# Optimization experiments

Hardware: AMD Instinct MI355X
Metric: run time of the kernel (lower is better)

The kernel has to match this reference:

```python
import jax, jax.numpy as jnp
import numpy as np
from jax import lax

B, C, H, W = 16, 3, 512, 512


def _nms(heat):
    # 3x3 max-pool, stride 1, SAME padding; keep only local peaks
    hmax = lax.reduce_window(heat, -jnp.inf, lax.max,
                             (1, 1, 3, 3), (1, 1, 1, 1), 'SAME')
    return heat * (hmax == heat).astype(heat.dtype)


def _topk(scores, K):
    b, c, h, w = scores.shape
    # per-class topk over the spatial plane
    topk_scores, topk_inds = lax.top_k(scores.reshape(b, c, h * w), K)  # [b,c,K]
    topk_row = (topk_inds // w).astype(scores.dtype)
    topk_col = (topk_inds % w).astype(scores.dtype)
    # global topk across (class, K)
    topk_score, topk_ind = lax.top_k(topk_scores.reshape(b, c * K), K)  # [b,K]
    topk_clses = topk_ind // K
    gath = lambda x: jnp.take_along_axis(x.reshape(b, c * K), topk_ind, axis=1)
    return topk_score, gath(topk_inds), topk_clses, gath(topk_row), gath(topk_col)


def _transpose_and_gather_feat(feat, inds):
    b, ch, h, w = feat.shape
    f = feat.transpose(0, 2, 3, 1).reshape(b, h * w, ch)  # [b,HW,ch]
    return jnp.take_along_axis(f, inds[:, :, None], axis=1)  # [b,K,ch]


def _decode(hm, cen_offset, direction, z_coor, dim, K):
    b = hm.shape[0]
    hm = _nms(hm)
    scores, inds, clses, row, col = _topk(hm, K)
    off = _transpose_and_gather_feat(cen_offset, inds)           # [b,K,2]
    col = col[:, :, None] + off[:, :, 0:1]
    row = row[:, :, None] + off[:, :, 1:2]
    direction = _transpose_and_gather_feat(direction, inds)      # [b,K,2]
    z_coor = _transpose_and_gather_feat(z_coor, inds)            # [b,K,1]
    dim = _transpose_and_gather_feat(dim, inds)                  # [b,K,3]
    clses = clses[:, :, None].astype(hm.dtype)
    scores = scores[:, :, None]
    return jnp.concatenate([scores, col, row, z_coor, dim, direction, clses], axis=2)


def setup_inputs() -> dict:
    key = jax.random.key(0)
    k1, k2, k3, k4, k5 = jax.random.split(key, 5)
    return {
        'hm_cen': jax.random.normal(k1, (B, C, H, W), jnp.float32),
        'cen_offset': jax.random.normal(k2, (B, 2, H, W), jnp.float32),
        'direction': jax.random.normal(k3, (B, 2, H, W), jnp.float32),
        'z_coor': jax.random.normal(k4, (B, 1, H, W), jnp.float32),
        'dim': jax.random.normal(k5, (B, 3, H, W), jnp.float32),
        'K': 500,
    }


def reference(hm_cen, cen_offset, direction, z_coor, dim, K):
    # postprocessing_v2 applies sigmoid to the class heatmap before decode
    heat = jax.nn.sigmoid(hm_cen)
    return _decode(heat, cen_offset, direction, z_coor, dim, K)  # [B,K,10]
```

## Files before the change

### kernel.cpp

```cpp
#include <hip/hip_runtime.h>
#include <math.h>
#include <float.h>

#define Hd 512
#define Wd 512
#define HWp (Hd*Wd)
#define Bn 16
#define Cn 3
#define NMAP (Bn*Cn)
#define KTOP 500
#define P_SPLIT 8
#define BAND 64
#define SCAP 4096

__device__ __forceinline__ uint32_t flipbits(float v){
  uint32_t u = __float_as_uint(v);
  return u ^ (0x80000000u | (uint32_t)(-(int32_t)(u>>31)));
}
__device__ __forceinline__ float unflipbits(uint32_t f){
  uint32_t u = f ^ ((f>>31)? 0x80000000u : 0xFFFFFFFFu);
  return __uint_as_float(u);
}

__device__ __forceinline__ void nms_row(
    const float4 p0, const float4 p1, const float4 c0, const float4 c1,
    const float4 n0, const float4 n1, const int lane,
    uint32_t& pk, float* cv)
{
  float vm0 = fmaxf(fmaxf(p0.x,c0.x),n0.x);
  float vm1 = fmaxf(fmaxf(p0.y,c0.y),n0.y);
  float vm2 = fmaxf(fmaxf(p0.z,c0.z),n0.z);
  float vm3 = fmaxf(fmaxf(p0.w,c0.w),n0.w);
  float vm4 = fmaxf(fmaxf(p1.x,c1.x),n1.x);
  float vm5 = fmaxf(fmaxf(p1.y,c1.y),n1.y);
  float vm6 = fmaxf(fmaxf(p1.z,c1.z),n1.z);
  float vm7 = fmaxf(fmaxf(p1.w,c1.w),n1.w);
  float vmL = __shfl_up(vm7, 1);   if (lane == 0)  vmL = -INFINITY;
  float vmR = __shfl_down(vm0, 1); if (lane == 63) vmR = -INFINITY;

  float m0 = fmaxf(vmL, fmaxf(vm0, vm1));
  float m1 = fmaxf(vm0, fmaxf(vm1, vm2));
  float m2 = fmaxf(vm1, fmaxf(vm2, vm3));
  float m3 = fmaxf(vm2, fmaxf(vm3, vm4));
  float m4 = fmaxf(vm3, fmaxf(vm4, vm5));
  float m5 = fmaxf(vm4, fmaxf(vm5, vm6));
  float m6 = fmaxf(vm5, fmaxf(vm6, vm7));
  float m7 = fmaxf(vm6, fmaxf(vm7, vmR));

  pk = 0;
  if (c0.x >= m0) pk |= 1u;
  if (c0.y >= m1) pk |= 2u;
  if (c0.z >= m2) pk |= 4u;
  if (c0.w >= m3) pk |= 8u;
  if (c1.x >= m4) pk |= 16u;
  if (c1.y >= m5) pk |= 32u;
  if (c1.z >= m6) pk |= 64u;
  if (c1.w >= m7) pk |= 128u;
  cv[0]=c0.x; cv[1]=c0.y; cv[2]=c0.z; cv[3]=c0.w;
  cv[4]=c1.x; cv[5]=c1.y; cv[6]=c1.z; cv[7]=c1.w;
}

__device__ __forceinline__ void append_row(
    const uint32_t pk, const float* cv, const uint32_t ibase,
    uint32_t* __restrict__ ctr, uint64_t* __restrict__ dst, const uint32_t cap,
    uint32_t* __restrict__ hist, const int lane)
{
  const uint32_t np = (uint32_t)__popc(pk);
  uint32_t incl = np;
  #pragma unroll
  for (int d = 1; d < 64; d <<= 1) { uint32_t u = __shfl_up(incl, d); if (lane >= d) incl += u; }
  const uint32_t tot = __shfl(incl, 63);
  if (!tot) return;
  uint32_t b0 = 0;
  if (lane == 0) b0 = atomicAdd(ctr, tot);
  b0 = __shfl(b0, 0);
  uint32_t pos = b0 + incl - np;
  #pragma unroll
  for (int i = 0; i < 8; ++i) {
    if ((pk >> i) & 1u) {
      const uint32_t fb = flipbits(cv[i]);
      if (pos < cap) dst[pos] = ((uint64_t)fb << 32) | (uint32_t)(~(ibase + (uint32_t)i));
      atomicAdd(&hist[fb >> 22], 1u);
      ++pos;
    }
  }
}

__device__ __forceinline__ void findT512(
    const uint32_t* hist, const uint32_t target, const int tid, const int lane,
    const int wid, uint32_t* wtot, uint32_t* res)
{
  const uint32_t s = hist[2*tid] + hist[2*tid+1];
  uint32_t v = s;
  #pragma unroll
  for (int d = 1; d < 64; d <<= 1) { uint32_t u = __shfl_down(v, d); if (lane + d < 64) v += u; }
  if (lane == 0) wtot[wid] = v;
  __syncthreads();
  uint32_t above = 0;
  for (int ww = wid + 1; ww < 8; ++ww) above += wtot[ww];
  const uint32_t gsuf = v + above;
  if (gsuf >= target && (gsuf - s) < target) {
    uint32_t cum = gsuf - s;
    for (int b = 2*tid + 1; b >= 2*tid; --b) {
      cum += hist[b];
      if (cum >= target) { res[0]=(uint32_t)b; res[1]=target-(cum-hist[b]); res[2]=cum; break; }
    }
  }
  __syncthreads();
}

__device__ __forceinline__ uint64_t cexch(uint64_t mine, uint64_t part, bool wantMax) {
  uint64_t mx = mine > part ? mine : part;
  uint64_t mn = mine > part ? part : mine;
  return wantMax ? mx : mn;
}

__device__ void bitonic512_reg(uint64_t& e0, uint64_t* sbuf, int tid, int lane)
{
  for (int k = 2; k <= 512; k <<= 1) {
    for (int j = k >> 1; j > 0; j >>= 1) {
      const bool up = ((tid & k) == 0);
      if (j >= 64) {
        __syncthreads();
        sbuf[tid] = e0;
        __syncthreads();
        uint64_t q = sbuf[tid ^ j];
        e0 = cexch(e0, q, up == ((tid & j) == 0));
      } else {
        uint64_t q = __shfl_xor((unsigned long long)e0, j);
        e0 = cexch(e0, q, up == ((lane & j) == 0));
      }
    }
  }
  __syncthreads();
  sbuf[tid] = e0;
  __syncthreads();
}

__device__ void sort1024_lds(uint64_t* a, int tid)
{
  for (int k = 2; k <= 1024; k <<= 1) {
    for (int j = k >> 1; j > 0; j >>= 1) {
      __syncthreads();
      const int lj = 31 - __clz(j);
      const int i  = ((tid >> lj) << (lj + 1)) | (tid & (j - 1));
      const int ixj = i | j;
      const uint64_t x = a[i], y = a[ixj];
      const bool up = ((i & k) == 0);
      const bool sw = up ? (x < y) : (x > y);
      if (sw) { a[i] = y; a[ixj] = x; }
    }
  }
  __syncthreads();
}

__global__ __launch_bounds__(512) void k_fused(
    const float* __restrict__ hm, uint64_t* __restrict__ l500)
{
  __shared__ uint64_t sbuf[SCAP];
  __shared__ uint32_t hist[1024];
  __shared__ uint32_t wtot[8];
  __shared__ uint32_t res[4];
  __shared__ uint32_t cnt1, cnt2;

  const int m = blockIdx.x >> 3, p = blockIdx.x & (P_SPLIT - 1);
  const int tid = threadIdx.x, lane = tid & 63, w = tid >> 6;
  const uint64_t lt = (1ull << lane) - 1ull;
  const float* map = hm + (size_t)m * HWp;
  const int xb = lane * 8;

  for (int i = tid; i < 1024; i += 512) hist[i] = 0;
  if (tid == 0) { cnt1 = 0; cnt2 = 0; }
  __syncthreads();

  const float4 NEG4 = make_float4(-INFINITY,-INFINITY,-INFINITY,-INFINITY);
  #pragma unroll
  for (int sub = 0; sub < 2; ++sub) {
    const int y0 = p * BAND + w * 8 + sub * 4;
    float4 ra[6], rb[6];
    #pragma unroll
    for (int r = 0; r < 6; ++r) {
      const int yy = y0 - 1 + r;
      if (yy >= 0 && yy < Hd) {
        const float* rp = map + (size_t)yy * Wd + xb;
        ra[r] = *(const float4*)rp; rb[r] = *(const float4*)(rp + 4);
      } else { ra[r] = NEG4; rb[r] = NEG4; }
    }
    #pragma unroll
    for (int r = 0; r < 4; ++r) {
      uint32_t pk; float cv[8];
      nms_row(ra[r], rb[r], ra[r+1], rb[r+1], ra[r+2], rb[r+2], lane, pk, cv);
      append_row(pk, cv, (uint32_t)((y0 + r) * Wd + xb), &cnt1, sbuf, (uint32_t)SCAP, hist, lane);
    }
  }
  __syncthreads();
  const uint32_t n = cnt1;
  const uint32_t nc = (n < (uint32_t)SCAP) ? n : (uint32_t)SCAP;

  uint32_t thresh20 = 0;
  if (n > 512) {
    findT512(hist, KTOP, tid, lane, w, wtot, res);
    const uint32_t T1 = res[0], krem = res[1];
    for (int i = tid; i < 1024; i += 512) hist[i] = 0;
    __syncthreads();
    #pragma unroll
    for (int s = 0; s < SCAP/512; ++s) {
      const uint32_t i = (uint32_t)tid + s * 512u;
      if (i < nc) {
        const uint32_t f = (uint32_t)(sbuf[i] >> 32);
        if ((f >> 22) == T1) atomicAdd(&hist[(f >> 12) & 1023u], 1u);
      }
    }
    __syncthreads();
    findT512(hist, krem, tid, lane, w, wtot, res);
    thresh20 = (T1 << 10) | res[0];
  }

  uint64_t sk0,sk1,sk2,sk3,sk4,sk5,sk6,sk7;
  bool kp0,kp1,kp2,kp3,kp4,kp5,kp6,kp7;
  {
    const uint32_t i0=(uint32_t)tid, i1=i0+512u, i2=i0+1024u, i3=i0+1536u,
                   i4=i0+2048u, i5=i0+2560u, i6=i0+3072u, i7=i0+3584u;
    sk0=sbuf[i0]; sk1=sbuf[i1]; sk2=sbuf[i2]; sk3=sbuf[i3];
    sk4=sbuf[i4]; sk5=sbuf[i5]; sk6=sbuf[i6]; sk7=sbuf[i7];
    kp0=(i0<nc)&&((uint32_t)(sk0>>44)>=thresh20);
    kp1=(i1<nc)&&((uint32_t)(sk1>>44)>=thresh20);
    kp2=(i2<nc)&&((uint32_t)(sk2>>44)>=thresh20);
    kp3=(i3<nc)&&((uint32_t)(sk3>>44)>=thresh20);
    kp4=(i4<nc)&&((uint32_t)(sk4>>44)>=thresh20);
    kp5=(i5<nc)&&((uint32_t)(sk5>>44)>=thresh20);
    kp6=(i6<nc)&&((uint32_t)(sk6>>44)>=thresh20);
    kp7=(i7<nc)&&((uint32_t)(sk7>>44)>=thresh20);
  }
  __syncthreads();
  #define APPEND1(SK, KP) {                                              \
    const unsigned long long mask = __ballot(KP);                        \
    if (mask) {                                                          \
      uint32_t b = 0;                                                    \
      if (lane == 0) b = atomicAdd(&cnt2, (uint32_t)__popcll(mask));     \
      b = __shfl(b, 0);                                                  \
      if (KP) {                                                          \
        const uint32_t pp = b + (uint32_t)__popcll(mask & lt);           \
        if (pp < 1024u) sbuf[pp] = SK;                                   \
      }                                                                  \
    }                                                                    \
  }
  APPEND1(sk0,kp0) APPEND1(sk1,kp1) APPEND1(sk2,kp2) APPEND1(sk3,kp3)
  APPEND1(sk4,kp4) APPEND1(sk5,kp5) APPEND1(sk6,kp6) APPEND1(sk7,kp7)
  #undef APPEND1
  __syncthreads();
  uint32_t M = cnt2; if (M > 1024u) M = 1024u;

  if (M <= 512u) {
    uint64_t e0 = (tid < (int)M) ? sbuf[tid] : 0ull;
    bitonic512_reg(e0, sbuf, tid, lane);
  } else {
    for (int i = (int)M + tid; i < 1024; i += 512) sbuf[i] = 0ull;
    sort1024_lds(sbuf, tid);
  }

  l500[(size_t)blockIdx.x * 512 + tid] = sbuf[tid];
}

__global__ __launch_bounds__(1024) void k_merge(
    const uint64_t* __restrict__ l500,
    float* __restrict__ s1_scores, uint32_t* __restrict__ s1_inds)
{
  __shared__ uint64_t ld[P_SPLIT * 512];
  const int m = blockIdx.x >> 1, h = blockIdx.x & 1;
  const int tid = threadIdx.x;
  const uint64_t* src = l500 + (size_t)m * (P_SPLIT * 512);
  for (int i = tid; i < P_SPLIT * 512; i += 1024) ld[i] = src[i];
  __syncthreads();

  #pragma unroll
  for (int e = 0; e < 2; ++e) {
    const int i = h * 2048 + e * 1024 + tid;
    const uint64_t kk = ld[i];
    const int r = i & 511, L = i >> 9;
    if (kk != 0ull && r < KTOP) {
      uint32_t pos[P_SPLIT - 1];
      #pragma unroll
      for (int d = 0; d < P_SPLIT - 1; ++d) pos[d] = 0;
      #pragma unroll
      for (int s = 512; s >= 1; s >>= 1) {
        #pragma unroll
        for (int d = 0; d < P_SPLIT - 1; ++d) {
          const uint64_t* lst = ld + (((L + 1 + d) & (P_SPLIT - 1)) << 9);
          const uint32_t idx = pos[d] + (uint32_t)s - 1u;
          const uint64_t v = (idx < 512u) ? lst[idx] : 0ull;
          if (v > kk) pos[d] += (uint32_t)s;
        }
      }
      uint32_t rank = (uint32_t)r;
      #pragma unroll
      for (int d = 0; d < P_SPLIT - 1; ++d) rank += pos[d];
      if (rank < KTOP) {
        const float v = unflipbits((uint32_t)(kk >> 32));
        s1_scores[m * 512 + rank] = 1.0f / (1.0f + expf(-v));
        s1_inds [m * 512 + rank] = ~(uint32_t)kk;
      }
    }
  }
}

__global__ __launch_bounds__(512) void k_final(
    const float* __restrict__ s1_scores, const uint32_t* __restrict__ s1_inds,
    const float* __restrict__ cen_offset, const float* __restrict__ direction,
    const float* __restrict__ z_coor, const float* __restrict__ dimf,
    float* __restrict__ out)
{
  __shared__ float ssc[Cn][KTOP];
  const int b = blockIdx.x / Cn, c = blockIdx.x % Cn;
  const int tid = threadIdx.x;

  for (int i = tid; i < Cn * KTOP; i += 512) {
    int cc = i / KTOP, r = i - cc * KTOP;
    ssc[cc][r] = s1_scores[(b * Cn + cc) * 512 + r];
  }
  __syncthreads();

  if (tid < KTOP) {
    const int r = tid;
    const int i = c * KTOP + r;
    const uint64_t mykey = ((uint64_t)flipbits(ssc[c][r]) << 32) | (uint32_t)(~(uint32_t)i);
    int rank = r;
    #pragma unroll
    for (int cd = 1; cd < Cn; ++cd) {
      const int cc = (c + cd) % Cn;
      int lo = 0, hi = KTOP;
      while (lo < hi) {
        int mid = (lo + hi) >> 1;
        uint64_t k2 = ((uint64_t)flipbits(ssc[cc][mid]) << 32)
                    | (uint32_t)(~(uint32_t)(cc * KTOP + mid));
        if (k2 > mykey) lo = mid + 1; else hi = mid;
      }
      rank += lo;
    }
    if (rank < KTOP) {
      const float* co = cen_offset + (size_t)b * 2 * HWp;
      const float* di = direction  + (size_t)b * 2 * HWp;
      const float* zc = z_coor     + (size_t)b * HWp;
      const float* dm = dimf       + (size_t)b * 3 * HWp;
      const int bcx = b * Cn + c;
      const uint32_t ind = s1_inds[bcx * 512 + r];
      float o[10];
      o[0] = ssc[c][r];
      o[1] = (float)(ind & (Wd - 1)) + co[ind];
      o[2] = (float)(ind >> 9) + co[HWp + ind];
      o[3] = zc[ind];
      o[4] = dm[ind];
      o[5] = dm[HWp + ind];
      o[6] = dm[2 * HWp + ind];
      o[7] = di[ind];
      o[8] = di[HWp + ind];
      o[9] = (float)c;
      float* op = out + ((size_t)b * KTOP + rank) * 10;
      #pragma unroll
      for (int q = 0; q < 10; ++q) op[q] = o[q];
    }
  }
}

extern "C" void kernel_launch(void* const* d_in, const int* in_sizes, int n_in,
                              void* d_out, int out_size, void* d_ws, size_t ws_size,
                              hipStream_t stream)
{
  const float* hm         = (const float*)d_in[0];
  const float* cen_offset = (const float*)d_in[1];
  const float* direction  = (const float*)d_in[2];
  const float* z_coor     = (const float*)d_in[3];
  const float* dimf       = (const float*)d_in[4];
  float* out = (float*)d_out;

  char* ws = (char*)d_ws;
  uint64_t* l500  = (uint64_t*)ws;
  size_t o1       = (size_t)NMAP * P_SPLIT * 512 * 8;
  float*    s1_sc = (float*)(ws + o1);
  uint32_t* s1_id = (uint32_t*)(ws + o1 + (size_t)NMAP * 512 * 4);

  k_fused<<<NMAP * P_SPLIT, 512, 0, stream>>>(hm, l500);
  k_merge<<<NMAP * 2, 1024, 0, stream>>>(l500, s1_sc, s1_id);
  k_final<<<Bn * Cn, 512, 0, stream>>>(s1_sc, s1_id, cen_offset, direction, z_coor, dimf, out);
}
```

Baseline: 51.43 us.

## Double k_fused block to 1024 threads and skip second histogram pass when possible

The fused NMS/top-k kernel now runs 1024 threads per block, each wave handling 4 rows instead of two 4-row sub-bands, which doubles the threads available to hide load latency. The threshold search can stop after the first 10-bit histogram when at most 1024 candidates survive. Otherwise a finer 12-bit second histogram is built. The candidate sort becomes a register/shuffle bitonic sort of up to 2048 elements, replacing the LDS-only 1024 sort. In exchange the block uses more shared memory (a 4096-bin histogram) and may sort larger candidate sets.

```diff
diff --git a/kernel.cpp b/kernel.cpp
--- a/kernel.cpp
+++ b/kernel.cpp
@@ -60,48 +60,41 @@
   cv[4]=c1.x; cv[5]=c1.y; cv[6]=c1.z; cv[7]=c1.w;
 }
 
-__device__ __forceinline__ void append_row(
-    const uint32_t pk, const float* cv, const uint32_t ibase,
-    uint32_t* __restrict__ ctr, uint64_t* __restrict__ dst, const uint32_t cap,
-    uint32_t* __restrict__ hist, const int lane)
-{
-  const uint32_t np = (uint32_t)__popc(pk);
-  uint32_t incl = np;
-  #pragma unroll
-  for (int d = 1; d < 64; d <<= 1) { uint32_t u = __shfl_up(incl, d); if (lane >= d) incl += u; }
-  const uint32_t tot = __shfl(incl, 63);
-  if (!tot) return;
-  uint32_t b0 = 0;
-  if (lane == 0) b0 = atomicAdd(ctr, tot);
-  b0 = __shfl(b0, 0);
-  uint32_t pos = b0 + incl - np;
-  #pragma unroll
-  for (int i = 0; i < 8; ++i) {
-    if ((pk >> i) & 1u) {
-      const uint32_t fb = flipbits(cv[i]);
-      if (pos < cap) dst[pos] = ((uint64_t)fb << 32) | (uint32_t)(~(ibase + (uint32_t)i));
-      atomicAdd(&hist[fb >> 22], 1u);
-      ++pos;
-    }
-  }
-}
-
-__device__ __forceinline__ void findT512(
+__device__ __forceinline__ void findT1024(
     const uint32_t* hist, const uint32_t target, const int tid, const int lane,
     const int wid, uint32_t* wtot, uint32_t* res)
 {
-  const uint32_t s = hist[2*tid] + hist[2*tid+1];
+  const uint32_t s = hist[tid];
   uint32_t v = s;
   #pragma unroll
   for (int d = 1; d < 64; d <<= 1) { uint32_t u = __shfl_down(v, d); if (lane + d < 64) v += u; }
   if (lane == 0) wtot[wid] = v;
   __syncthreads();
   uint32_t above = 0;
-  for (int ww = wid + 1; ww < 8; ++ww) above += wtot[ww];
+  for (int ww = wid + 1; ww < 16; ++ww) above += wtot[ww];
+  const uint32_t gsuf = v + above;
+  if (gsuf >= target && (gsuf - s) < target) {
+    res[0] = (uint32_t)tid; res[1] = target - (gsuf - s); res[2] = gsuf;
+  }
+  __syncthreads();
+}
+
+__device__ __forceinline__ void findT4096(
+    const uint32_t* hist, const uint32_t target, const int tid, const int lane,
+    const int wid, uint32_t* wtot, uint32_t* res)
+{
+  const uint32_t s = hist[4*tid] + hist[4*tid+1] + hist[4*tid+2] + hist[4*tid+3];
+  uint32_t v = s;
+  #pragma unroll
+  for (int d = 1; d < 64; d <<= 1) { uint32_t u = __shfl_down(v, d); if (lane + d < 64) v += u; }
+  if (lane == 0) wtot[wid] = v;
+  __syncthreads();
+  uint32_t above = 0;
+  for (int ww = wid + 1; ww < 16; ++ww) above += wtot[ww];
   const uint32_t gsuf = v + above;
   if (gsuf >= target && (gsuf - s) < target) {
     uint32_t cum = gsuf - s;
-    for (int b = 2*tid + 1; b >= 2*tid; --b) {
+    for (int b = 4*tid + 3; b >= 4*tid; --b) {
       cum += hist[b];
       if (cum >= target) { res[0]=(uint32_t)b; res[1]=target-(cum-hist[b]); res[2]=cum; break; }
     }
@@ -115,9 +108,9 @@
   return wantMax ? mx : mn;
 }
 
-__device__ void bitonic512_reg(uint64_t& e0, uint64_t* sbuf, int tid, int lane)
-{
-  for (int k = 2; k <= 512; k <<= 1) {
+__device__ void bitonic1024_1t(uint64_t& e0, uint64_t* sbuf, int tid, int lane)
+{
+  for (int k = 2; k <= 1024; k <<= 1) {
     for (int j = k >> 1; j > 0; j >>= 1) {
       const bool up = ((tid & k) == 0);
       if (j >= 64) {
@@ -137,29 +130,44 @@
   __syncthreads();
 }
 
-__device__ void sort1024_lds(uint64_t* a, int tid)
-{
-  for (int k = 2; k <= 1024; k <<= 1) {
+__device__ void bitonic2048_reg(uint64_t& e0, uint64_t& e1, uint64_t* sbuf, int tid, int lane)
+{
+  const int i1 = tid + 1024;
+  for (int k = 2; k <= 2048; k <<= 1) {
     for (int j = k >> 1; j > 0; j >>= 1) {
-      __syncthreads();
-      const int lj = 31 - __clz(j);
-      const int i  = ((tid >> lj) << (lj + 1)) | (tid & (j - 1));
-      const int ixj = i | j;
-      const uint64_t x = a[i], y = a[ixj];
-      const bool up = ((i & k) == 0);
-      const bool sw = up ? (x < y) : (x > y);
-      if (sw) { a[i] = y; a[ixj] = x; }
-    }
-  }
-  __syncthreads();
-}
-
-__global__ __launch_bounds__(512) void k_fused(
+      if (j >= 1024) {
+        uint64_t mx = e0 > e1 ? e0 : e1;
+        uint64_t mn = e0 > e1 ? e1 : e0;
+        e0 = mx; e1 = mn;
+      } else if (j >= 64) {
+        __syncthreads();
+        sbuf[tid] = e0; sbuf[i1] = e1;
+        __syncthreads();
+        uint64_t q0 = sbuf[tid ^ j];
+        uint64_t q1 = sbuf[i1 ^ j];
+        bool amS = ((tid & j) == 0);
+        e0 = cexch(e0, q0, ((tid & k) == 0) == amS);
+        e1 = cexch(e1, q1, ((i1  & k) == 0) == amS);
+      } else {
+        uint64_t q0 = __shfl_xor((unsigned long long)e0, j);
+        uint64_t q1 = __shfl_xor((unsigned long long)e1, j);
+        bool amS = ((lane & j) == 0);
+        e0 = cexch(e0, q0, ((tid & k) == 0) == amS);
+        e1 = cexch(e1, q1, ((i1  & k) == 0) == amS);
+      }
+    }
+  }
+  __syncthreads();
+  sbuf[tid] = e0; sbuf[i1] = e1;
+  __syncthreads();
+}
+
+__global__ __launch_bounds__(1024) void k_fused(
     const float* __restrict__ hm, uint64_t* __restrict__ l500)
 {
   __shared__ uint64_t sbuf[SCAP];
-  __shared__ uint32_t hist[1024];
-  __shared__ uint32_t wtot[8];
+  __shared__ uint32_t hist[4096];
+  __shared__ uint32_t wtot[16];
   __shared__ uint32_t res[4];
   __shared__ uint32_t cnt1, cnt2;
 
@@ -167,70 +175,88 @@
   const int tid = threadIdx.x, lane = tid & 63, w = tid >> 6;
   const uint64_t lt = (1ull << lane) - 1ull;
   const float* map = hm + (size_t)m * HWp;
+  const int y0 = p * BAND + w * 4;
   const int xb = lane * 8;
 
-  for (int i = tid; i < 1024; i += 512) hist[i] = 0;
+  if (tid < 1024) hist[tid] = 0;
   if (tid == 0) { cnt1 = 0; cnt2 = 0; }
   __syncthreads();
 
   const float4 NEG4 = make_float4(-INFINITY,-INFINITY,-INFINITY,-INFINITY);
+  float4 ra[6], rb[6];
   #pragma unroll
-  for (int sub = 0; sub < 2; ++sub) {
-    const int y0 = p * BAND + w * 8 + sub * 4;
-    float4 ra[6], rb[6];
+  for (int r = 0; r < 6; ++r) {
+    const int yy = y0 - 1 + r;
+    if (yy >= 0 && yy < Hd) {
+      const float* rp = map + (size_t)yy * Wd + xb;
+      ra[r] = *(const float4*)rp; rb[r] = *(const float4*)(rp + 4);
+    } else { ra[r] = NEG4; rb[r] = NEG4; }
+  }
+
+  #pragma unroll
+  for (int r = 0; r < 4; ++r) {
+    uint32_t pk; float cv[8];
+    nms_row(ra[r], rb[r], ra[r+1], rb[r+1], ra[r+2], rb[r+2], lane, pk, cv);
+    const uint32_t np = (uint32_t)__popc(pk);
+    uint32_t incl = np;
     #pragma unroll
-    for (int r = 0; r < 6; ++r) {
-      const int yy = y0 - 1 + r;
-      if (yy >= 0 && yy < Hd) {
-        const float* rp = map + (size_t)yy * Wd + xb;
-        ra[r] = *(const float4*)rp; rb[r] = *(const float4*)(rp + 4);
-      } else { ra[r] = NEG4; rb[r] = NEG4; }
-    }
+    for (int d = 1; d < 64; d <<= 1) { uint32_t u = __shfl_up(incl, d); if (lane >= d) incl += u; }
+    const uint32_t tot = __shfl(incl, 63);
+    if (!tot) continue;
+    uint32_t b0 = 0;
+    if (lane == 0) b0 = atomicAdd(&cnt1, tot);
+    b0 = __shfl(b0, 0);
+    uint32_t pos = b0 + incl - np;
+    const uint32_t ib = (uint32_t)((y0 + r) * Wd + xb);
     #pragma unroll
-    for (int r = 0; r < 4; ++r) {
-      uint32_t pk; float cv[8];
-      nms_row(ra[r], rb[r], ra[r+1], rb[r+1], ra[r+2], rb[r+2], lane, pk, cv);
-      append_row(pk, cv, (uint32_t)((y0 + r) * Wd + xb), &cnt1, sbuf, (uint32_t)SCAP, hist, lane);
+    for (int i = 0; i < 8; ++i) {
+      if ((pk >> i) & 1u) {
+        const uint32_t fb = flipbits(cv[i]);
+        if (pos < (uint32_t)SCAP)
+          sbuf[pos] = ((uint64_t)fb << 32) | (uint32_t)(~(ib + (uint32_t)i));
+        atomicAdd(&hist[fb >> 22], 1u);
+        ++pos;
+      }
     }
   }
   __syncthreads();
   const uint32_t n = cnt1;
   const uint32_t nc = (n < (uint32_t)SCAP) ? n : (uint32_t)SCAP;
 
-  uint32_t thresh20 = 0;
+  uint32_t shift = 22, thr = 0;
   if (n > 512) {
-    findT512(hist, KTOP, tid, lane, w, wtot, res);
-    const uint32_t T1 = res[0], krem = res[1];
-    for (int i = tid; i < 1024; i += 512) hist[i] = 0;
+    findT1024(hist, KTOP, tid, lane, w, wtot, res);
+    const uint32_t T1 = res[0], krem = res[1], M0 = res[2];
     __syncthreads();
-    #pragma unroll
-    for (int s = 0; s < SCAP/512; ++s) {
-      const uint32_t i = (uint32_t)tid + s * 512u;
-      if (i < nc) {
-        const uint32_t f = (uint32_t)(sbuf[i] >> 32);
-        if ((f >> 22) == T1) atomicAdd(&hist[(f >> 12) & 1023u], 1u);
-      }
-    }
-    __syncthreads();
-    findT512(hist, krem, tid, lane, w, wtot, res);
-    thresh20 = (T1 << 10) | res[0];
-  }
-
-  uint64_t sk0,sk1,sk2,sk3,sk4,sk5,sk6,sk7;
-  bool kp0,kp1,kp2,kp3,kp4,kp5,kp6,kp7;
+    if (M0 <= 1024u) {
+      thr = T1;
+    } else {
+      for (int i = tid; i < 4096; i += 1024) hist[i] = 0;
+      __syncthreads();
+      #pragma unroll
+      for (int s = 0; s < SCAP/1024; ++s) {
+        const uint32_t i = (uint32_t)tid + s * 1024u;
+        if (i < nc) {
+          const uint32_t f = (uint32_t)(sbuf[i] >> 32);
+          if ((f >> 22) == T1) atomicAdd(&hist[(f >> 10) & 4095u], 1u);
+        }
+      }
+      __syncthreads();
+      findT4096(hist, krem, tid, lane, w, wtot, res);
+      shift = 10; thr = (T1 << 12) | res[0];
+      __syncthreads();
+    }
+  }
+
+  uint64_t sk0, sk1, sk2, sk3;
+  bool kp0, kp1, kp2, kp3;
   {
-    const uint32_t i0=(uint32_t)tid, i1=i0+512u, i2=i0+1024u, i3=i0+1536u,
-                   i4=i0+2048u, i5=i0+2560u, i6=i0+3072u, i7=i0+3584u;
-    sk0=sbuf[i0]; sk1=sbuf[i1]; sk2=sbuf[i2]; sk3=sbuf[i3];
-    sk4=sbuf[i4]; sk5=sbuf[i5]; sk6=sbuf[i6]; sk7=sbuf[i7];
-    kp0=(i0<nc)&&((uint32_t)(sk0>>44)>=thresh20);
-    kp1=(i1<nc)&&((uint32_t)(sk1>>44)>=thresh20);
-    kp2=(i2<nc)&&((uint32_t)(sk2>>44)>=thresh20);
-    kp3=(i3<nc)&&((uint32_t)(sk3>>44)>=thresh20);
-    kp4=(i4<nc)&&((uint32_t)(sk4>>44)>=thresh20);
-    kp5=(i5<nc)&&((uint32_t)(sk5>>44)>=thresh20);
-    kp6=(i6<nc)&&((uint32_t)(sk6>>44)>=thresh20);
-    kp7=(i7<nc)&&((uint32_t)(sk7>>44)>=thresh20);
+    const uint32_t i0 = (uint32_t)tid, i1 = i0 + 1024u, i2 = i0 + 2048u, i3 = i0 + 3072u;
+    sk0 = sbuf[i0]; sk1 = sbuf[i1]; sk2 = sbuf[i2]; sk3 = sbuf[i3];
+    kp0 = (i0 < nc) && (((uint32_t)(sk0 >> 32) >> shift) >= thr);
+    kp1 = (i1 < nc) && (((uint32_t)(sk1 >> 32) >> shift) >= thr);
+    kp2 = (i2 < nc) && (((uint32_t)(sk2 >> 32) >> shift) >= thr);
+    kp3 = (i3 < nc) && (((uint32_t)(sk3 >> 32) >> shift) >= thr);
   }
   __syncthreads();
   #define APPEND1(SK, KP) {                                              \
@@ -241,25 +267,27 @@
       b = __shfl(b, 0);                                                  \
       if (KP) {                                                          \
         const uint32_t pp = b + (uint32_t)__popcll(mask & lt);           \
-        if (pp < 1024u) sbuf[pp] = SK;                                   \
+        if (pp < 2048u) sbuf[pp] = SK;                                   \
       }                                                                  \
     }                                                                    \
   }
-  APPEND1(sk0,kp0) APPEND1(sk1,kp1) APPEND1(sk2,kp2) APPEND1(sk3,kp3)
-  APPEND1(sk4,kp4) APPEND1(sk5,kp5) APPEND1(sk6,kp6) APPEND1(sk7,kp7)
+  APPEND1(sk0, kp0) APPEND1(sk1, kp1) APPEND1(sk2, kp2) APPEND1(sk3, kp3)
   #undef APPEND1
   __syncthreads();
-  uint32_t M = cnt2; if (M > 1024u) M = 1024u;
-
-  if (M <= 512u) {
-    uint64_t e0 = (tid < (int)M) ? sbuf[tid] : 0ull;
-    bitonic512_reg(e0, sbuf, tid, lane);
+  uint32_t M = cnt2; if (M > 2048u) M = 2048u;
+  for (uint32_t i = M + (uint32_t)tid; i < 2048u; i += 1024u) sbuf[i] = 0ull;
+  __syncthreads();
+
+  if (M <= 1024u) {
+    uint64_t e0 = sbuf[tid];
+    bitonic1024_1t(e0, sbuf, tid, lane);
   } else {
-    for (int i = (int)M + tid; i < 1024; i += 512) sbuf[i] = 0ull;
-    sort1024_lds(sbuf, tid);
-  }
-
-  l500[(size_t)blockIdx.x * 512 + tid] = sbuf[tid];
+    uint64_t e0 = sbuf[tid], e1 = sbuf[tid + 1024];
+    bitonic2048_reg(e0, e1, sbuf, tid, lane);
+  }
+
+  if (tid < 512)
+    l500[(size_t)blockIdx.x * 512 + tid] = sbuf[tid];
 }
 
 __global__ __launch_bounds__(1024) void k_merge(
@@ -379,7 +407,7 @@
   float*    s1_sc = (float*)(ws + o1);
   uint32_t* s1_id = (uint32_t*)(ws + o1 + (size_t)NMAP * 512 * 4);
 
-  k_fused<<<NMAP * P_SPLIT, 512, 0, stream>>>(hm, l500);
-  k_merge<<<NMAP * 2, 1024, 0, stream>>>(l500, s1_sc, s1_id);
-  k_final<<<Bn * Cn, 512, 0, stream>>>(s1_sc, s1_id, cen_offset, direction, z_coor, dimf, out);
-}
+  k_fused<<<NMAP * P_SPLIT, 1024, 0, stream>>>(hm, l500);
+  k_merge<<<NMAP * 2,       1024, 0, stream>>>(l500, s1_sc, s1_id);
+  k_final<<<Bn * Cn,         512, 0, stream>>>(s1_sc, s1_id, cen_offset, direction, z_coor, dimf, out);
+}
```

Result: slower. 64.51 us (+25.4%).
